# Kernel tuning notes

Measured on AMD Instinct MI355X. Metric: run time of the kernel, lower is better.

The kernel has to match this reference:

```python
import jax, jax.numpy as jnp
import numpy as np

B, N, K, L, H = 8, 2048, 16, 4, 8
CONV = (64, 64, 128, 256)
W_DIM, N_CODES, E_DIM, P_DIM, FF = 512, 8, 64, 256, 512


def act(x):
    return jax.nn.leaky_relu(x, 0.2)


def ln(x, g, b, eps=1e-5):
    m = jnp.mean(x, -1, keepdims=True)
    v = jnp.mean((x - m) ** 2, -1, keepdims=True)
    return g * (x - m) / jnp.sqrt(v + eps) + b


# per-batch neighbor gather: f [C,N], i [N,K] -> [C,N,K]
gather_nb = jax.vmap(lambda f, i: f[:, i])


def knn_idx(y):  # y [B,3,N] -> [B,N,K]
    xx = jnp.sum(y * y, axis=1)
    inner = jnp.einsum('bcn,bcm->bnm', y, y)
    dist = 2.0 * inner - xx[:, :, None] - xx[:, None, :]  # negative sq dist
    return jax.lax.top_k(dist, K)[1]


def mha(q, kv, Wq, bq, Wk, bk, Wv, bv, Wo, bo):
    Bq, S, D = q.shape
    Sk = kv.shape[1]
    dh = D // H
    qh = (q @ Wq.T + bq).reshape(Bq, S, H, dh)
    kh = (kv @ Wk.T + bk).reshape(Bq, Sk, H, dh)
    vh = (kv @ Wv.T + bv).reshape(Bq, Sk, H, dh)
    a = jax.nn.softmax(jnp.einsum('bqhd,bkhd->bhqk', qh, kh) * (1.0 / np.sqrt(dh)))
    o = jnp.einsum('bhqk,bkhd->bqhd', a, vh).reshape(Bq, S, D)
    return o @ Wo.T + bo


def setup_inputs() -> dict:
    key = jax.random.key(0)
    ks = iter(jax.random.split(key, 48))
    nrm = lambda shape: jax.random.normal(next(ks), shape, jnp.float32) * 0.02
    d = {
        'x': jax.random.normal(next(ks), (B, N, 3), jnp.float32),
        'W_ec': nrm((CONV[0], 6)), 'b_ec': jnp.zeros((CONV[0],), jnp.float32),
        'Wc1': nrm((CONV[1], CONV[0])), 'bc1': jnp.zeros((CONV[1],), jnp.float32),
        'Wc2': nrm((CONV[2], CONV[1])), 'bc2': jnp.zeros((CONV[2],), jnp.float32),
        'Wc3': nrm((CONV[3], CONV[2])), 'bc3': jnp.zeros((CONV[3],), jnp.float32),
        'Wf': nrm((W_DIM, sum(CONV))), 'bf': jnp.zeros((W_DIM,), jnp.float32),
        'Wpc': nrm((P_DIM, E_DIM)), 'bpc': jnp.zeros((P_DIM,), jnp.float32),
        'Wpi': nrm((P_DIM, 3)), 'bpi': jnp.zeros((P_DIM,), jnp.float32),
        'Wq': nrm((L, 2, P_DIM, P_DIM)), 'bq': jnp.zeros((L, 2, P_DIM), jnp.float32),
        'Wk': nrm((L, 2, P_DIM, P_DIM)), 'bk': jnp.zeros((L, 2, P_DIM), jnp.float32),
        'Wv': nrm((L, 2, P_DIM, P_DIM)), 'bv': jnp.zeros((L, 2, P_DIM), jnp.float32),
        'Wo': nrm((L, 2, P_DIM, P_DIM)), 'bo': jnp.zeros((L, 2, P_DIM), jnp.float32),
        'ln1g': jnp.ones((L, P_DIM), jnp.float32), 'ln1b': jnp.zeros((L, P_DIM), jnp.float32),
        'ln2g': jnp.ones((L, P_DIM), jnp.float32), 'ln2b': jnp.zeros((L, P_DIM), jnp.float32),
        'Wff1': nrm((L, FF, P_DIM)), 'bff1': jnp.zeros((L, FF), jnp.float32),
        'Wff2': nrm((L, P_DIM, FF)), 'bff2': jnp.zeros((L, P_DIM), jnp.float32),
        'ln3g': jnp.ones((L, P_DIM), jnp.float32), 'ln3b': jnp.zeros((L, P_DIM), jnp.float32),
        'lnfg': jnp.ones((P_DIM,), jnp.float32), 'lnfb': jnp.zeros((P_DIM,), jnp.float32),
        'Wcm': nrm((E_DIM, P_DIM)), 'bcm': jnp.zeros((E_DIM,), jnp.float32),
    }
    return d


def reference(x, W_ec, b_ec, Wc1, bc1, Wc2, bc2, Wc3, bc3, Wf, bf, Wpc, bpc, Wpi, bpi,
              Wq, bq, Wk, bk, Wv, bv, Wo, bo, ln1g, ln1b, ln2g, ln2b,
              Wff1, bff1, Wff2, bff2, ln3g, ln3b, lnfg, lnfb, Wcm, bcm):
    y = jnp.transpose(x, (0, 2, 1))                      # [B,3,N]
    idx = knn_idx(y)                                     # [B,N,K]
    nb = gather_nb(y, idx)                               # [B,3,N,K]
    feats = jnp.concatenate([nb - y[..., None], jnp.broadcast_to(y[..., None], nb.shape)], axis=1)
    h = act(jnp.einsum('oc,bcnk->bonk', W_ec, feats) + b_ec[:, None, None])
    h = h.max(axis=3)                                    # [B,64,N]
    xs = [h]
    for Wl, bl in ((Wc1, bc1), (Wc2, bc2), (Wc3, bc3)):
        h = gather_nb(h, idx).max(axis=3)                # graph max pooling
        h = act(jnp.einsum('oc,bcn->bon', Wl, h) + bl[:, None])
        xs.append(h)
    h = jnp.concatenate(xs, axis=1)                      # [B,512,N]
    h = jnp.einsum('oc,bcn->bon', Wf, h) + bf[:, None]
    xm = h.max(axis=2)                                   # [B,512]
    q = act(xm.reshape(B, N_CODES, E_DIM) @ Wpc.T + bpc) # [B,8,256]
    mem = act(x @ Wpi.T + bpi)                           # [B,N,256]
    for l in range(L):
        q = ln(q + mha(q, q, Wq[l, 0], bq[l, 0], Wk[l, 0], bk[l, 0], Wv[l, 0], bv[l, 0], Wo[l, 0], bo[l, 0]), ln1g[l], ln1b[l])
        q = ln(q + mha(q, mem, Wq[l, 1], bq[l, 1], Wk[l, 1], bk[l, 1], Wv[l, 1], bv[l, 1], Wo[l, 1], bo[l, 1]), ln2g[l], ln2b[l])
        q = ln(q + (act(q @ Wff1[l].T + bff1[l]) @ Wff2[l].T + bff2[l]), ln3g[l], ln3b[l])
    q = ln(q, lnfg, lnfb)
    out = q @ Wcm.T + bcm                                # [B,8,64]
    return out.reshape(B, W_DIM)
```

## Files before the change

### kernel.cpp

```cpp
#include <hip/hip_runtime.h>
#include <math.h>

#define BN 8
#define NP 2048
#define KNN 16
#define NL 4
#define NH 8

typedef __attribute__((ext_vector_type(8))) short bf16x8;
typedef __attribute__((ext_vector_type(4))) float f32x4;

__device__ __forceinline__ unsigned short f2bf(float f) {
    unsigned u = __float_as_uint(f);
    unsigned r = (u + 0x7FFFu + ((u >> 16) & 1u)) >> 16;
    return (unsigned short)r;
}
__device__ __forceinline__ float bf2f(unsigned short s) {
    return __uint_as_float(((unsigned)s) << 16);
}
__device__ __forceinline__ unsigned fmono(float f) {
    unsigned u = __float_as_uint(f);
    return (u & 0x80000000u) ? ~u : (u | 0x80000000u);
}
__device__ __forceinline__ float funmono(unsigned k) {
    return (k & 0x80000000u) ? __uint_as_float(k ^ 0x80000000u) : __uint_as_float(~k);
}


__device__ __forceinline__ unsigned long long shflx_u64(unsigned long long v, int j) {
    int lo = __shfl_xor((int)(unsigned)(v & 0xFFFFFFFFull), j);
    int hi = __shfl_xor((int)(unsigned)(v >> 32), j);
    return ((unsigned long long)(unsigned)hi << 32) | (unsigned)lo;
}

__device__ __forceinline__ unsigned sort64_u32(unsigned v, int lane) {
    #pragma unroll
    for (int k = 2; k <= 64; k <<= 1) {
        #pragma unroll
        for (int j = k >> 1; j > 0; j >>= 1) {
            unsigned o = (unsigned)__shfl_xor((int)v, j);
            bool up = ((lane & k) == 0);
            bool lower = ((lane & j) == 0);
            unsigned mn = v < o ? v : o;
            unsigned mx = v < o ? o : v;
            v = (up == lower) ? mn : mx;
        }
    }
    return v;
}

__device__ __forceinline__ unsigned long long sort64_u64(unsigned long long v, int lane) {
    #pragma unroll
    for (int k = 2; k <= 64; k <<= 1) {
        #pragma unroll
        for (int j = k >> 1; j > 0; j >>= 1) {
            unsigned long long o = shflx_u64(v, j);
            bool up = ((lane & k) == 0);
            bool lower = ((lane & j) == 0);
            unsigned long long mn = v < o ? v : o;
            unsigned long long mx = v < o ? o : v;
            v = (up == lower) ? mn : mx;
        }
    }
    return v;
}

__global__ __launch_bounds__(256) void knn_kernel(const float* __restrict__ x, int* __restrict__ idxout) {
    __shared__ unsigned long long cand[4][64];
    int tid = threadIdx.x;
    int wv = tid >> 6, lane = tid & 63;
    int p = blockIdx.x * 4 + wv;
    int b = p >> 11, n = p & 2047;
    const float* xb = x + (size_t)b * NP * 3;
    float cx = xb[n * 3 + 0], cy = xb[n * 3 + 1], cz = xb[n * 3 + 2];
    float xn = cx * cx + cy * cy + cz * cz;
    unsigned key[32];
    unsigned lmax = 0u;
    #pragma unroll
    for (int t = 0; t < 32; ++t) {
        int m = (t << 6) | lane;
        float mx = xb[m * 3 + 0], my = xb[m * 3 + 1], mz = xb[m * 3 + 2];
        float xxm = mx * mx + my * my + mz * mz;
        float inner = cx * mx + cy * my + cz * mz;
        float dd = 2.0f * inner - xn - xxm;
        unsigned u = __float_as_uint(dd);
        u = (u & 0x80000000u) ? ~u : (u | 0x80000000u);
        key[t] = u;
        lmax = lmax > u ? lmax : u;
    }
    unsigned sorted = sort64_u32(lmax, lane);
    unsigned S = (unsigned)__shfl((int)sorted, 48);
    int c = 0;
    #pragma unroll
    for (int t = 0; t < 32; ++t) c += (key[t] >= S) ? 1 : 0;
    int inc = c;
    #pragma unroll
    for (int d = 1; d < 64; d <<= 1) {
        int tsh = __shfl_up(inc, d);
        if (lane >= d) inc += tsh;
    }
    int C = __shfl(inc, 63);
    int* op = idxout + (size_t)p * KNN;
    if (C <= 64) {
        int off = inc - c;
        #pragma unroll
        for (int t = 0; t < 32; ++t) {
            if (key[t] >= S) {
                int m = (t << 6) | lane;
                cand[wv][off++] = ((unsigned long long)key[t] << 16) | (unsigned)(2047 - m);
            }
        }
        asm volatile("s_waitcnt lgkmcnt(0)" ::: "memory");
        unsigned long long ck = (lane < C) ? cand[wv][lane] : 0ull;
        ck = sort64_u64(ck, lane);
        if (lane >= 48) op[63 - lane] = 2047 - (int)(unsigned)(ck & 0xFFFFull);
    } else {
        unsigned taken = 0u;
        for (int r = 0; r < KNN; ++r) {
            unsigned long long best = 0ull;
            #pragma unroll
            for (int t = 0; t < 32; ++t) {
                if (!((taken >> t) & 1u)) {
                    int m = (t << 6) | lane;
                    unsigned long long ck = ((unsigned long long)key[t] << 16) | (unsigned)(2047 - m);
                    if (ck > best) best = ck;
                }
            }
            #pragma unroll
            for (int d = 1; d < 64; d <<= 1) {
                unsigned long long o = shflx_u64(best, d);
                if (o > best) best = o;
            }
            int m = 2047 - (int)(unsigned)(best & 0xFFFFull);
            if (lane == 0) op[r] = m;
            if ((m & 63) == lane) taken |= 1u << (m >> 6);
        }
    }
}

__global__ __launch_bounds__(256) void edge_conv_kernel(const float* __restrict__ x, const int* __restrict__ idx,
                                                        const float* __restrict__ Wec, const float* __restrict__ bec,
                                                        unsigned short* __restrict__ hcatT) {
    int tid = threadIdx.x;
    int g = tid >> 6, o = tid & 63;
    int p = blockIdx.x * 4 + g;
    int b = p >> 11;
    __shared__ float nb[4][KNN][3];
    __shared__ float ctr[4][3];
    if (o < KNN) {
        int j = idx[(size_t)p * KNN + o];
        const float* xp = x + ((size_t)b * NP + j) * 3;
        nb[g][o][0] = xp[0]; nb[g][o][1] = xp[1]; nb[g][o][2] = xp[2];
    }
    if (o >= KNN && o < KNN + 3) ctr[g][o - KNN] = x[(size_t)p * 3 + (o - KNN)];
    __syncthreads();
    float w0 = Wec[o * 6 + 0], w1 = Wec[o * 6 + 1], w2 = Wec[o * 6 + 2];
    float w3 = Wec[o * 6 + 3], w4 = Wec[o * 6 + 4], w5 = Wec[o * 6 + 5];
    float c0 = ctr[g][0], c1 = ctr[g][1], c2 = ctr[g][2];
    float base = bec[o] + w3 * c0 + w4 * c1 + w5 * c2;
    float m = -3.4e38f;
    #pragma unroll
    for (int k = 0; k < KNN; ++k) {
        float v = base + w0 * (nb[g][k][0] - c0) + w1 * (nb[g][k][1] - c1) + w2 * (nb[g][k][2] - c2);
        v = v > 0.f ? v : 0.2f * v;
        m = fmaxf(m, v);
    }
    hcatT[(size_t)p * 512 + o] = f2bf(m);
}

__global__ __launch_bounds__(256) void pool_bf16_kernel(const unsigned short* __restrict__ src, int s_coff,
                                                        const int* __restrict__ idx,
                                                        unsigned short* __restrict__ dst, int C) {
    int tid = threadIdx.x, wv = tid >> 6, lane = tid & 63;
    int p = blockIdx.x * 4 + wv;
    int b = p >> 11;
    const int* ip = idx + (size_t)p * KNN;
    const unsigned short* sb = src + (size_t)b * NP * 512 + s_coff;
    for (int c0 = 0; c0 < C; c0 += 64) {
        int ch = c0 + lane;
        float m = -3.4e38f;
// ... 102 lines not shown
                                                        const unsigned short* __restrict__ B, size_t b_bstride,
                                                        const float* __restrict__ bias, int bias_per_m,
                                                        void* __restrict__ C, size_t c_bstride, int c_rstride,
                                                        int K, int act, int out_bf16,
                                                        unsigned* __restrict__ xmk, int domax) {
    __shared__ unsigned short As[128][40];
    __shared__ unsigned short Bs[128][40];
    int m0 = blockIdx.x * 128, n0 = blockIdx.y * 128, b = blockIdx.z;
    int tid = threadIdx.x;
    int lane = tid & 63, wave = tid >> 6;
    int wr = wave >> 1, wc = wave & 1;
    int quad = lane >> 4, l16 = lane & 15;
    int r0 = tid >> 2, kc0 = (tid & 3) * 8;
    f32x4 acc[4][4] = {};
    const unsigned short* Ab = A + (size_t)b * a_bstride;
    const unsigned short* Bb = B + (size_t)b * b_bstride;
    for (int k0 = 0; k0 < K; k0 += 32) {
        uint4 a0 = *(const uint4*)(Ab + (size_t)(m0 + r0) * K + k0 + kc0);
        uint4 a1 = *(const uint4*)(Ab + (size_t)(m0 + r0 + 64) * K + k0 + kc0);
        uint4 b0 = *(const uint4*)(Bb + (size_t)(n0 + r0) * K + k0 + kc0);
        uint4 b1 = *(const uint4*)(Bb + (size_t)(n0 + r0 + 64) * K + k0 + kc0);
        __syncthreads();
        *(uint4*)&As[r0][kc0] = a0;
        *(uint4*)&As[r0 + 64][kc0] = a1;
        *(uint4*)&Bs[r0][kc0] = b0;
        *(uint4*)&Bs[r0 + 64][kc0] = b1;
        __syncthreads();
        bf16x8 af[4], bfv[4];
        #pragma unroll
        for (int i = 0; i < 4; ++i) af[i] = *(const bf16x8*)&As[wr * 64 + i * 16 + l16][quad * 8];
        #pragma unroll
        for (int j = 0; j < 4; ++j) bfv[j] = *(const bf16x8*)&Bs[wc * 64 + j * 16 + l16][quad * 8];
        #pragma unroll
        for (int i = 0; i < 4; ++i)
            #pragma unroll
            for (int j = 0; j < 4; ++j)
                acc[i][j] = __builtin_amdgcn_mfma_f32_16x16x32_bf16(af[i], bfv[j], acc[i][j], 0, 0, 0);
    }
    if (domax) {
        #pragma unroll
        for (int i = 0; i < 4; ++i) {
            #pragma unroll
            for (int r = 0; r < 4; ++r) {
                int m = m0 + wr * 64 + i * 16 + quad * 4 + r;
                float v = fmaxf(fmaxf(acc[i][0][r], acc[i][1][r]), fmaxf(acc[i][2][r], acc[i][3][r]));
                v += bias[m];
                #pragma unroll
                for (int off = 1; off <= 8; off <<= 1) v = fmaxf(v, __shfl_xor(v, off));
                if (l16 == 0) atomicMax(&xmk[(size_t)b * 512 + m], fmono(v));
            }
        }
        return;
    }
    #pragma unroll
    for (int i = 0; i < 4; ++i) {
        #pragma unroll
        for (int r = 0; r < 4; ++r) {
            int m = m0 + wr * 64 + i * 16 + quad * 4 + r;
            float bm = bias_per_m ? bias[m] : 0.f;
            #pragma unroll
            for (int j = 0; j < 4; ++j) {
                int n = n0 + wc * 64 + j * 16 + l16;
                float v = acc[i][j][r] + (bias_per_m ? bm : bias[n]);
                if (act) v = v > 0.f ? v : 0.2f * v;
                size_t off = (size_t)b * c_bstride + (size_t)m * c_rstride + n;
                if (out_bf16) ((unsigned short*)C)[off] = f2bf(v);
                else          ((float*)C)[off] = v;
            }
        }
    }
}

__global__ __launch_bounds__(256) void mfma_kv_all_kernel(const unsigned short* __restrict__ A,
                                                          const unsigned short* __restrict__ W,
                                                          const float* __restrict__ bkv,
                                                          unsigned short* __restrict__ KVall) {
    __shared__ unsigned short As[128][40];
    __shared__ unsigned short Bs[128][40];
    int m0 = blockIdx.x * 128;
    int nb = blockIdx.y & 3, l = blockIdx.y >> 2;
    int n0 = nb * 128;
    int b = blockIdx.z;
    int tid = threadIdx.x;
    int lane = tid & 63, wave = tid >> 6;
    int wr = wave >> 1, wc = wave & 1;
    int quad = lane >> 4, l16 = lane & 15;
    int r0 = tid >> 2, kc0 = (tid & 3) * 8;
    f32x4 acc[4][4] = {};
    const unsigned short* Ab = A + (size_t)b * NP * 256;
    const unsigned short* Bb = W + (size_t)l * 131072;
    const float* bias = bkv + l * 512;
    for (int k0 = 0; k0 < 256; k0 += 32) {
        uint4 a0 = *(const uint4*)(Ab + (size_t)(m0 + r0) * 256 + k0 + kc0);
        uint4 a1 = *(const uint4*)(Ab + (size_t)(m0 + r0 + 64) * 256 + k0 + kc0);
        uint4 b0 = *(const uint4*)(Bb + (size_t)(n0 + r0) * 256 + k0 + kc0);
        uint4 b1 = *(const uint4*)(Bb + (size_t)(n0 + r0 + 64) * 256 + k0 + kc0);
        __syncthreads();
        *(uint4*)&As[r0][kc0] = a0;
        *(uint4*)&As[r0 + 64][kc0] = a1;
        *(uint4*)&Bs[r0][kc0] = b0;
        *(uint4*)&Bs[r0 + 64][kc0] = b1;
        __syncthreads();
        bf16x8 af[4], bfv[4];
        #pragma unroll
        for (int i = 0; i < 4; ++i) af[i] = *(const bf16x8*)&As[wr * 64 + i * 16 + l16][quad * 8];
        #pragma unroll
        for (int j = 0; j < 4; ++j) bfv[j] = *(const bf16x8*)&Bs[wc * 64 + j * 16 + l16][quad * 8];
        #pragma unroll
        for (int i = 0; i < 4; ++i)
            #pragma unroll
            for (int j = 0; j < 4; ++j)
                acc[i][j] = __builtin_amdgcn_mfma_f32_16x16x32_bf16(af[i], bfv[j], acc[i][j], 0, 0, 0);
    }
    unsigned short* Cb = KVall + ((size_t)l * BN + b) * NP * 512;
    #pragma unroll
    for (int i = 0; i < 4; ++i) {
        #pragma unroll
        for (int r = 0; r < 4; ++r) {
            int m = m0 + wr * 64 + i * 16 + quad * 4 + r;
            #pragma unroll
            for (int j = 0; j < 4; ++j) {
                int n = n0 + wc * 64 + j * 16 + l16;
                Cb[(size_t)m * 512 + n] = f2bf(acc[i][j][r] + bias[n]);
            }
        }
    }
}

__global__ __launch_bounds__(256) void pc_kernel(const unsigned* __restrict__ xmk, const float* __restrict__ Wpc,
                                                 const float* __restrict__ bpc, float* __restrict__ q) {
    int id = blockIdx.x * 256 + threadIdx.x;
    int p = id & 255;
    int rowi = id >> 8;
    int b = rowi >> 3, i = rowi & 7;
    const unsigned* xr = xmk + b * 512 + i * 64;
    const float* w = Wpc + (size_t)p * 64;
    float acc = bpc[p];
    #pragma unroll
    for (int e = 0; e < 64; ++e) acc += funmono(xr[e]) * w[e];
    q[id] = acc > 0.f ? acc : 0.2f * acc;
}

__global__ __launch_bounds__(256) void mem_kernel(const float* __restrict__ x, const float* __restrict__ Wpi,
                                                  const float* __restrict__ bpi, unsigned short* __restrict__ memB) {
    size_t id = (size_t)blockIdx.x * 256 + threadIdx.x;
    int p = (int)(id & 255);
    size_t pt = id >> 8;
    float x0 = x[pt * 3 + 0], x1 = x[pt * 3 + 1], x2 = x[pt * 3 + 2];
    float v = bpi[p] + x0 * Wpi[p * 3 + 0] + x1 * Wpi[p * 3 + 1] + x2 * Wpi[p * 3 + 2];
    v = v > 0.f ? v : 0.2f * v;
    memB[id] = f2bf(v);
}

__global__ __launch_bounds__(256) void qkv_proj_kernel(const float* __restrict__ in,
                                                       const float* __restrict__ Wq0, const float* __restrict__ bq0,
                                                       const float* __restrict__ Wk0, const float* __restrict__ bk0,
                                                       const float* __restrict__ Wv0, const float* __restrict__ bv0,
                                                       float* __restrict__ Qs, float* __restrict__ Ks,
                                                       float* __restrict__ Vs) {
    int which = blockIdx.y;
    const float* W = (which == 0) ? Wq0 : (which == 1) ? Wk0 : Wv0;
    const float* bb = (which == 0) ? bq0 : (which == 1) ? bk0 : bv0;
    float* out = (which == 0) ? Qs : (which == 1) ? Ks : Vs;
    __shared__ __align__(16) float r[256];
    int row = blockIdx.x, tid = threadIdx.x;
    r[tid] = in[(size_t)row * 256 + tid];
    __syncthreads();
    const float4* w4 = (const float4*)(W + (size_t)tid * 256);
    const float4* r4 = (const float4*)r;
    float acc = bb[tid];
    #pragma unroll 8
    for (int c = 0; c < 64; ++c) {
        float4 a = r4[c], wv = w4[c];
        acc += a.x * wv.x + a.y * wv.y + a.z * wv.z + a.w * wv.w;
    }
    out[(size_t)row * 256 + tid] = acc;
}

__global__ __launch_bounds__(256) void attn_ln_kernel(const float* __restrict__ Qs, const float* __restrict__ Ks,
                                                      const float* __restrict__ Vs, const float* __restrict__ Wo,
                                                      const float* __restrict__ bo, const float* __restrict__ res,
                                                      const float* __restrict__ g, const float* __restrict__ bt,
                                                      const float* __restrict__ Wq1, const float* __restrict__ bq1,
                                                      float* __restrict__ out, float* __restrict__ Qc) {
    int row = blockIdx.x, tid = threadIdx.x;
    int b = row >> 3;
    __shared__ float Kl[2048], Vl[2048], qr[256];
    __shared__ float sc[64];
    __shared__ __align__(16) float r[256];
    __shared__ __align__(16) float aout[256];
    __shared__ float red[256];
    for (int t = tid; t < 2048; t += 256) {
        Kl[t] = Ks[(size_t)b * 2048 + t];
        Vl[t] = Vs[(size_t)b * 2048 + t];
    }
    qr[tid] = Qs[(size_t)row * 256 + tid];
    __syncthreads();
    const float scale = 0.17677669529663687f;
    if (tid < 64) {
        int h = tid >> 3, k = tid & 7;
        float dot = 0.f;
        #pragma unroll
        for (int d = 0; d < 32; ++d) dot += qr[h * 32 + d] * Kl[k * 256 + h * 32 + d];
        sc[tid] = dot * scale;
    }
    __syncthreads();
    if (tid < 8) {
        float* p = sc + tid * 8;
        float m = -3.4e38f;
        #pragma unroll
        for (int k = 0; k < 8; ++k) m = fmaxf(m, p[k]);
        float s = 0.f;
        #pragma unroll
        for (int k = 0; k < 8; ++k) { p[k] = __expf(p[k] - m); s += p[k]; }
        float inv = 1.f / s;
        #pragma unroll
        for (int k = 0; k < 8; ++k) p[k] *= inv;
    }
    __syncthreads();
    {
        int h = tid >> 5;
        float acc = 0.f;
        #pragma unroll
        for (int k = 0; k < 8; ++k) acc += sc[h * 8 + k] * Vl[k * 256 + tid];
        r[tid] = acc;
    }
    __syncthreads();
    const float4* w4 = (const float4*)(Wo + (size_t)tid * 256);
    const float4* r4 = (const float4*)r;
    float acc = bo[tid];
    #pragma unroll 8
    for (int c = 0; c < 64; ++c) {
        float4 a = r4[c], wv = w4[c];
        acc += a.x * wv.x + a.y * wv.y + a.z * wv.z + a.w * wv.w;
    }
    float v = res[(size_t)row * 256 + tid] + acc;
    red[tid] = v; __syncthreads();
    for (int s = 128; s; s >>= 1) { if (tid < s) red[tid] += red[tid + s]; __syncthreads(); }
    float mean = red[0] * (1.0f / 256.0f);
    __syncthreads();
    float dv = v - mean;
    red[tid] = dv * dv; __syncthreads();
    for (int s = 128; s; s >>= 1) { if (tid < s) red[tid] += red[tid + s]; __syncthreads(); }
    float var = red[0] * (1.0f / 256.0f);
    float oln = g[tid] * dv * rsqrtf(var + 1e-5f) + bt[tid];
    out[(size_t)row * 256 + tid] = oln;
    aout[tid] = oln;
    __syncthreads();
    {
        const float4* wq4 = (const float4*)(Wq1 + (size_t)tid * 256);
        const float4* a4 = (const float4*)aout;
        float qacc = bq1[tid];
        #pragma unroll 8
        for (int c = 0; c < 64; ++c) {
            float4 a = a4[c], wv = wq4[c];
            qacc += a.x * wv.x + a.y * wv.y + a.z * wv.z + a.w * wv.w;
        }
        Qc[(size_t)row * 256 + tid] = qacc;
    }
}

__global__ __launch_bounds__(256) void ca_part_kernel(const float* __restrict__ Qc,
                                                      const unsigned short* __restrict__ KVl,
                                                      float* __restrict__ part) {
    int kb = blockIdx.x, h = blockIdx.y, b = blockIdx.z;
    int tid = threadIdx.x;
    __shared__ float q[8][32];
    __shared__ __align__(16) float S[8][128];
    __shared__ float om[8][8][32];
    const float scale = 0.17677669529663687f;
    {
        int i = tid >> 5, d = tid & 31;
        q[i][d] = Qc[(size_t)(b * 8 + i) * 256 + h * 32 + d];
    }
    __syncthreads();
    {
        int kk = tid & 127, half = tid >> 7;
        int k = kb * 128 + kk;
        const unsigned short* kp = KVl + ((size_t)b * NP + k) * 512 + h * 32;
        float kd[32];
        #pragma unroll
        for (int u = 0; u < 4; ++u) {
            uint4 raw = *(const uint4*)(kp + u * 8);
            unsigned w0 = raw.x, w1 = raw.y, w2 = raw.z, w3 = raw.w;
            kd[u * 8 + 0] = __uint_as_float(w0 << 16); kd[u * 8 + 1] = __uint_as_float(w0 & 0xFFFF0000u);
            kd[u * 8 + 2] = __uint_as_float(w1 << 16); kd[u * 8 + 3] = __uint_as_float(w1 & 0xFFFF0000u);
            kd[u * 8 + 4] = __uint_as_float(w2 << 16); kd[u * 8 + 5] = __uint_as_float(w2 & 0xFFFF0000u);
            kd[u * 8 + 6] = __uint_as_float(w3 << 16); kd[u * 8 + 7] = __uint_as_float(w3 & 0xFFFF0000u);
        }
        #pragma unroll
        for (int i = 0; i < 4; ++i) {
            int ri = half * 4 + i;
            float dot = 0.f;
            #pragma unroll
            for (int d = 0; d < 32; ++d) dot += q[ri][d] * kd[d];
            S[ri][kk] = dot * scale;
        }
    }
    __syncthreads();
    float* pout = part + (((size_t)(b * NH + h)) * 16 + kb) * 288;
    {
        int i = tid >> 5, l32 = tid & 31;
        float m = -3.4e38f;
        #pragma unroll
        for (int t = 0; t < 4; ++t) m = fmaxf(m, S[i][l32 + t * 32]);
        #pragma unroll
        for (int off = 16; off; off >>= 1) m = fmaxf(m, __shfl_xor(m, off));
        float s = 0.f;
        #pragma unroll
        for (int t = 0; t < 4; ++t) {
            float e = __expf(S[i][l32 + t * 32] - m);
            S[i][l32 + t * 32] = e;
            s += e;
        }
        #pragma unroll
        for (int off = 16; off; off >>= 1) s += __shfl_xor(s, off);
        if (l32 == 0) { pout[i] = m; pout[8 + i] = s; }
    }
    __syncthreads();
    {
        int d = tid & 31, grp = tid >> 5;
        const unsigned short* Vb = KVl + ((size_t)b * NP + kb * 128) * 512 + 256 + h * 32 + d;
        float acc[8] = {};
        #pragma unroll 4
        for (int t = 0; t < 16; ++t) {
            int kk = grp * 16 + t;
            float v = bf2f(Vb[(size_t)kk * 512]);
            #pragma unroll
            for (int i = 0; i < 8; ++i) acc[i] += S[i][kk] * v;
        }
        #pragma unroll
        for (int i = 0; i < 8; ++i) om[grp][i][d] = acc[i];
    }
    __syncthreads();
    {
        int i = tid >> 5, d = tid & 31;
        float sum = 0.f;
        #pragma unroll
        for (int g = 0; g < 8; ++g) sum += om[g][i][d];
        pout[16 + i * 32 + d] = sum;
    }
}

__global__ __launch_bounds__(256) void combine_ff_kernel(const float* __restrict__ part, const float* __restrict__ Wo,
                                                         const float* __restrict__ bo, const float* __restrict__ res,
                                                         const float* __restrict__ g2, const float* __restrict__ b2t,
                                                         const float* __restrict__ W1, const float* __restrict__ b1,
                                                         const float* __restrict__ W2, const float* __restrict__ b2,
                                                         const float* __restrict__ g3, const float* __restrict__ b3t,
                                                         float* __restrict__ out,
                                                         int is_last, const float* __restrict__ lnfg,
                                                         const float* __restrict__ lnfb, const float* __restrict__ Wcm,
                                                         const float* __restrict__ bcm, float* __restrict__ finout) {
    int row = blockIdx.x, tid = threadIdx.x;
    int b = row >> 3, i = row & 7;
    __shared__ __align__(16) float r[256];
    __shared__ __align__(16) float a[256];
    __shared__ __align__(16) float hbuf[512];
    __shared__ float red[256];
    {
        int h = tid >> 5, d = tid & 31;
        const float* pb = part + (size_t)(b * NH + h) * 16 * 288;
        float M = -3.4e38f;
        #pragma unroll
        for (int kb = 0; kb < 16; ++kb) M = fmaxf(M, pb[kb * 288 + i]);
        float L = 0.f, O = 0.f;
        #pragma unroll
        for (int kb = 0; kb < 16; ++kb) {
            float w = __expf(pb[kb * 288 + i] - M);
            L += pb[kb * 288 + 8 + i] * w;
            O += pb[kb * 288 + 16 + i * 32 + d] * w;
        }
        r[tid] = O / L;
    }
    __syncthreads();
    {
        const float4* w4 = (const float4*)(Wo + (size_t)tid * 256);
        const float4* r4 = (const float4*)r;
        float acc = bo[tid];
        #pragma unroll 8
        for (int c = 0; c < 64; ++c) {
            float4 av = r4[c], wv = w4[c];
            acc += av.x * wv.x + av.y * wv.y + av.z * wv.z + av.w * wv.w;
        }
        float v = res[(size_t)row * 256 + tid] + acc;
        red[tid] = v; __syncthreads();
        for (int s = 128; s; s >>= 1) { if (tid < s) red[tid] += red[tid + s]; __syncthreads(); }
        float mean = red[0] * (1.0f / 256.0f);
        __syncthreads();
        float dv = v - mean;
        red[tid] = dv * dv; __syncthreads();
        for (int s = 128; s; s >>= 1) { if (tid < s) red[tid] += red[tid + s]; __syncthreads(); }
        float var = red[0] * (1.0f / 256.0f);
        a[tid] = g2[tid] * dv * rsqrtf(var + 1e-5f) + b2t[tid];
    }
    __syncthreads();
    {
        const float4* a4 = (const float4*)a;
        #pragma unroll
        for (int half = 0; half < 2; ++half) {
            int o = tid + half * 256;
            const float4* w4 = (const float4*)(W1 + (size_t)o * 256);
            float acc = b1[o];
            #pragma unroll 8
            for (int c = 0; c < 64; ++c) {
                float4 av = a4[c], wv = w4[c];
                acc += av.x * wv.x + av.y * wv.y + av.z * wv.z + av.w * wv.w;
            }
            hbuf[o] = acc > 0.f ? acc : 0.2f * acc;
        }
    }
    __syncthreads();
    float tln;
    {
        const float4* h4 = (const float4*)hbuf;
        const float4* w4 = (const float4*)(W2 + (size_t)tid * 512);
        float acc = b2[tid];
        #pragma unroll 8
        for (int c = 0; c < 128; ++c) {
            float4 av = h4[c], wv = w4[c];
            acc += av.x * wv.x + av.y * wv.y + av.z * wv.z + av.w * wv.w;
        }
        float v = a[tid] + acc;
        red[tid] = v; __syncthreads();
        for (int s = 128; s; s >>= 1) { if (tid < s) red[tid] += red[tid + s]; __syncthreads(); }
        float mean = red[0] * (1.0f / 256.0f);
        __syncthreads();
        float dv = v - mean;
        red[tid] = dv * dv; __syncthreads();
        for (int s = 128; s; s >>= 1) { if (tid < s) red[tid] += red[tid + s]; __syncthreads(); }
        float var = red[0] * (1.0f / 256.0f);
        tln = g3[tid] * dv * rsqrtf(var + 1e-5f) + b3t[tid];
    }
    if (!is_last) {
        out[(size_t)row * 256 + tid] = tln;
        return;
    }
    __syncthreads();
    red[tid] = tln; __syncthreads();
    for (int s = 128; s; s >>= 1) { if (tid < s) red[tid] += red[tid + s]; __syncthreads(); }
    float mean = red[0] * (1.0f / 256.0f);
    __syncthreads();
    float dv = tln - mean;
    red[tid] = dv * dv; __syncthreads();
    for (int s = 128; s; s >>= 1) { if (tid < s) red[tid] += red[tid + s]; __syncthreads(); }
    float var = red[0] * (1.0f / 256.0f);
    a[tid] = lnfg[tid] * dv * rsqrtf(var + 1e-5f) + lnfb[tid];
    __syncthreads();
    if (tid < 64) {
        const float4* w4 = (const float4*)(Wcm + (size_t)tid * 256);
        const float4* a4 = (const float4*)a;
        float acc = bcm[tid];
        #pragma unroll 8
        for (int c = 0; c < 64; ++c) {
            float4 av = a4[c], wv = w4[c];
            acc += av.x * wv.x + av.y * wv.y + av.z * wv.z + av.w * wv.w;
        }
        finout[(size_t)b * 512 + i * 64 + tid] = acc;
    }
}

extern "C" void kernel_launch(void* const* d_in, const int* in_sizes, int n_in,
                              void* d_out, int out_size, void* d_ws, size_t ws_size,
                              hipStream_t stream) {
    const float* x    = (const float*)d_in[0];
    const float* Wec  = (const float*)d_in[1];
    const float* bec  = (const float*)d_in[2];
    const float* Wc1  = (const float*)d_in[3];
    const float* bc1  = (const float*)d_in[4];
    const float* Wc2  = (const float*)d_in[5];
    const float* bc2  = (const float*)d_in[6];
    const float* Wc3  = (const float*)d_in[7];
    const float* bc3  = (const float*)d_in[8];
    const float* Wf   = (const float*)d_in[9];
    const float* bf   = (const float*)d_in[10];
    const float* Wpc  = (const float*)d_in[11];
    const float* bpc  = (const float*)d_in[12];
    const float* Wpi  = (const float*)d_in[13];
    const float* bpi  = (const float*)d_in[14];
    const float* Wq   = (const float*)d_in[15];
    const float* bq   = (const float*)d_in[16];
    const float* Wk   = (const float*)d_in[17];
    const float* bk   = (const float*)d_in[18];
    const float* Wv   = (const float*)d_in[19];
    const float* bv   = (const float*)d_in[20];
    const float* Wo   = (const float*)d_in[21];
    const float* bo   = (const float*)d_in[22];
    const float* ln1g = (const float*)d_in[23];
    const float* ln1b = (const float*)d_in[24];
    const float* ln2g = (const float*)d_in[25];
    const float* ln2b = (const float*)d_in[26];
    const float* Wff1 = (const float*)d_in[27];
    const float* bff1 = (const float*)d_in[28];
    const float* Wff2 = (const float*)d_in[29];
    const float* bff2 = (const float*)d_in[30];
    const float* ln3g = (const float*)d_in[31];
    const float* ln3b = (const float*)d_in[32];
    const float* lnfg = (const float*)d_in[33];
    const float* lnfb = (const float*)d_in[34];
    const float* Wcm  = (const float*)d_in[35];
    const float* bcm  = (const float*)d_in[36];
    float* out = (float*)d_out;

    float* ws = (float*)d_ws;
    size_t off = 0;
    auto alloc = [&](size_t n) { float* p = ws + off; off += (n + 3) & ~(size_t)3; return p; };
    int*            idx   = (int*)alloc((size_t)BN * NP * KNN);
    unsigned short* hcatT = (unsigned short*)alloc((size_t)BN * NP * 512 / 2);
    unsigned short* poolT = (unsigned short*)alloc((size_t)BN * NP * 128 / 2);
    unsigned short* WfB   = (unsigned short*)alloc(262144 / 2);
    unsigned short* Wc1B  = (unsigned short*)alloc(4096 / 2);
    unsigned short* Wc2B  = (unsigned short*)alloc(8192 / 2);
    unsigned short* Wc3B  = (unsigned short*)alloc(32768 / 2);
    unsigned short* WkvB  = (unsigned short*)alloc(524288 / 2);
    float*          bkv   = alloc(2048);
    unsigned short* memB  = (unsigned short*)alloc((size_t)BN * NP * 256 / 2);
    unsigned short* KVall = (unsigned short*)alloc((size_t)NL * BN * NP * 512 / 2);
    unsigned*       xmk   = (unsigned*)alloc((size_t)BN * 512);
    float*          qa    = alloc((size_t)BN * 8 * 256);
    float*          qb    = alloc((size_t)BN * 8 * 256);
    float*          Qs    = alloc((size_t)BN * 8 * 256);
    float*          Ks    = alloc((size_t)BN * 8 * 256);
    float*          Vs    = alloc((size_t)BN * 8 * 256);
    float*          Qc    = alloc((size_t)BN * 8 * 256);
    float*          part  = alloc((size_t)BN * NH * 16 * 288);

    wcast_kernel<<<3272, 256, 0, stream>>>(Wf, Wc3, Wk, Wv, bk, bv, Wc1, Wc2,
                                           WfB, Wc3B, WkvB, bkv, Wc1B, Wc2B, xmk);

    knn_kernel<<<BN * NP / 4, 256, 0, stream>>>(x, idx);
    edge_conv_kernel<<<BN * NP / 4, 256, 0, stream>>>(x, idx, Wec, bec, hcatT);

    pool_bf16_kernel<<<BN * NP / 4, 256, 0, stream>>>(hcatT, 0, idx, poolT, 64);
    mfma_conv64_kernel<<<dim3(NP / 128, 1, BN), 256, 0, stream>>>(poolT, Wc1B, bc1, hcatT, 64);
    pool_bf16_kernel<<<BN * NP / 4, 256, 0, stream>>>(hcatT, 64, idx, poolT, 64);
    mfma_gemm_kernel<<<dim3(NP / 128, 1, BN), 256, 0, stream>>>(poolT, (size_t)NP * 64, Wc2B, 0,
                                                                bc2, 0, (void*)(hcatT + 128), (size_t)NP * 512, 512,
                                                                64, 1, 1, nullptr, 0);
    pool_bf16_kernel<<<BN * NP / 4, 256, 0, stream>>>(hcatT, 128, idx, poolT, 128);
    mfma_gemm_kernel<<<dim3(NP / 128, 2, BN), 256, 0, stream>>>(poolT, (size_t)NP * 128, Wc3B, 0,
                                                                bc3, 0, (void*)(hcatT + 256), (size_t)NP * 512, 512,
                                                                128, 1, 1, nullptr, 0);
    mfma_gemm_kernel<<<dim3(4, NP / 128, BN), 256, 0, stream>>>(WfB, 0, hcatT, (size_t)NP * 512,
                                                                bf, 1, nullptr, 0, 0,
                                                                512, 0, 0, xmk, 1);
    pc_kernel<<<BN * 8, 256, 0, stream>>>(xmk, Wpc, bpc, qa);
    mem_kernel<<<BN * NP, 256, 0, stream>>>(x, Wpi, bpi, memB);
    mfma_kv_all_kernel<<<dim3(NP / 128, 4 * NL, BN), 256, 0, stream>>>(memB, WkvB, bkv, KVall);

    float* qcur = qa; float* qnxt = qb;
    for (int l = 0; l < NL; ++l) {
        const float* Wq0 = Wq + (size_t)(l * 2 + 0) * 65536; const float* bq0 = bq + (l * 2 + 0) * 256;
        const float* Wk0 = Wk + (size_t)(l * 2 + 0) * 65536; const float* bk0 = bk + (l * 2 + 0) * 256;
        const float* Wv0 = Wv + (size_t)(l * 2 + 0) * 65536; const float* bv0 = bv + (l * 2 + 0) * 256;
        const float* Wo0 = Wo + (size_t)(l * 2 + 0) * 65536; const float* bo0 = bo + (l * 2 + 0) * 256;
        const float* Wq1 = Wq + (size_t)(l * 2 + 1) * 65536; const float* bq1 = bq + (l * 2 + 1) * 256;
        const float* Wo1 = Wo + (size_t)(l * 2 + 1) * 65536; const float* bo1 = bo + (l * 2 + 1) * 256;
        int last = (l == NL - 1);

        qkv_proj_kernel<<<dim3(BN * 8, 3), 256, 0, stream>>>(qcur, Wq0, bq0, Wk0, bk0, Wv0, bv0, Qs, Ks, Vs);
        attn_ln_kernel<<<BN * 8, 256, 0, stream>>>(Qs, Ks, Vs, Wo0, bo0, qcur,
                                                   ln1g + l * 256, ln1b + l * 256, Wq1, bq1, qnxt, Qc);
        ca_part_kernel<<<dim3(16, NH, BN), 256, 0, stream>>>(Qc, KVall + (size_t)l * BN * NP * 512, part);
        combine_ff_kernel<<<BN * 8, 256, 0, stream>>>(part, Wo1, bo1, qnxt,
                                                      ln2g + l * 256, ln2b + l * 256,
                                                      Wff1 + (size_t)l * 512 * 256, bff1 + l * 512,
                                                      Wff2 + (size_t)l * 256 * 512, bff2 + l * 256,
                                                      ln3g + l * 256, ln3b + l * 256, qcur,
                                                      last, lnfg, lnfb, Wcm, bcm, out);
    }

    (void)in_sizes; (void)n_in; (void)out_size; (void)ws_size; (void)qnxt;
}
```

Baseline: 615.6 us.

## Restructure transformer tail into split-bf16 MFMA GEMM kernels with LN folding

Replaces the per-row scalar matvec kernels of the decoder (QKV projection, attention plus LN, combine plus FFN) with a generic 64-row MFMA GEMM kernel. The kernel uses a hi/lo bf16 split to keep near-fp32 accuracy and folds the preceding LayerNorm into its input load. Each weight matrix is now read once per panel instead of once per row, which cuts the redundant weight traffic of the 64-block matvec design. The cost is many more small launches per layer (about eight instead of four), each using only 4-12 blocks, plus extra global round trips for intermediates.

```diff
diff --git a/kernel.cpp b/kernel.cpp
--- a/kernel.cpp
+++ b/kernel.cpp
@@ -9,6 +9,7 @@
 
 typedef __attribute__((ext_vector_type(8))) short bf16x8;
 typedef __attribute__((ext_vector_type(4))) float f32x4;
+typedef __attribute__((ext_vector_type(4))) unsigned short us4;
 
 __device__ __forceinline__ unsigned short f2bf(float f) {
     unsigned u = __float_as_uint(f);
@@ -25,7 +26,6 @@
 __device__ __forceinline__ float funmono(unsigned k) {
     return (k & 0x80000000u) ? __uint_as_float(k ^ 0x80000000u) : __uint_as_float(~k);
 }
-
 
 __device__ __forceinline__ unsigned long long shflx_u64(unsigned long long v, int j) {
     int lo = __shfl_xor((int)(unsigned)(v & 0xFFFFFFFFull), j);
@@ -434,61 +434,150 @@
     memB[id] = f2bf(v);
 }
 
-__global__ __launch_bounds__(256) void qkv_proj_kernel(const float* __restrict__ in,
-                                                       const float* __restrict__ Wq0, const float* __restrict__ bq0,
-                                                       const float* __restrict__ Wk0, const float* __restrict__ bk0,
-                                                       const float* __restrict__ Wv0, const float* __restrict__ bv0,
-                                                       float* __restrict__ Qs, float* __restrict__ Ks,
-                                                       float* __restrict__ Vs) {
-    int which = blockIdx.y;
-    const float* W = (which == 0) ? Wq0 : (which == 1) ? Wk0 : Wv0;
-    const float* bb = (which == 0) ? bq0 : (which == 1) ? bk0 : bv0;
-    float* out = (which == 0) ? Qs : (which == 1) ? Ks : Vs;
-    __shared__ __align__(16) float r[256];
-    int row = blockIdx.x, tid = threadIdx.x;
-    r[tid] = in[(size_t)row * 256 + tid];
-    __syncthreads();
-    const float4* w4 = (const float4*)(W + (size_t)tid * 256);
-    const float4* r4 = (const float4*)r;
-    float acc = bb[tid];
-    #pragma unroll 8
-    for (int c = 0; c < 64; ++c) {
-        float4 a = r4[c], wv = w4[c];
-        acc += a.x * wv.x + a.y * wv.y + a.z * wv.z + a.w * wv.w;
-    }
-    out[(size_t)row * 256 + tid] = acc;
-}
-
-__global__ __launch_bounds__(256) void attn_ln_kernel(const float* __restrict__ Qs, const float* __restrict__ Ks,
-                                                      const float* __restrict__ Vs, const float* __restrict__ Wo,
-                                                      const float* __restrict__ bo, const float* __restrict__ res,
-                                                      const float* __restrict__ g, const float* __restrict__ bt,
-                                                      const float* __restrict__ Wq1, const float* __restrict__ bq1,
-                                                      float* __restrict__ out, float* __restrict__ Qc) {
-    int row = blockIdx.x, tid = threadIdx.x;
-    int b = row >> 3;
-    __shared__ float Kl[2048], Vl[2048], qr[256];
-    __shared__ float sc[64];
-    __shared__ __align__(16) float r[256];
-    __shared__ __align__(16) float aout[256];
-    __shared__ float red[256];
-    for (int t = tid; t < 2048; t += 256) {
-        Kl[t] = Ks[(size_t)b * 2048 + t];
-        Vl[t] = Vs[(size_t)b * 2048 + t];
-    }
-    qr[tid] = Qs[(size_t)row * 256 + tid];
+__global__ __launch_bounds__(256) void tail_gemm_kernel(
+    const float* __restrict__ in, int K, int nk,
+    const float* __restrict__ Wa, const float* __restrict__ Wb2, const float* __restrict__ Wc2,
+    const float* __restrict__ ba, const float* __restrict__ bb2, const float* __restrict__ bc2,
+    const float* __restrict__ resid,
+    const float* __restrict__ lng, const float* __restrict__ lnb, float* __restrict__ lnout,
+    float* __restrict__ out, int N, int act)
+{
+    __shared__ unsigned short Ah[64][72], Al[64][72];
+    __shared__ unsigned short Bh[64][72], Bl[64][72];
+    __shared__ float meanv[64], rsv[64];
+    int panel = blockIdx.x;
+    int tid = threadIdx.x;
+    int lane = tid & 63, w = tid >> 6;
+    int quad = lane >> 4, l16 = lane & 15;
+    int grp = panel >> 2;
+    const float* W = (grp == 0) ? Wa : (grp == 1) ? Wb2 : Wc2;
+    const float* bi = (grp == 0) ? ba : (grp == 1) ? bb2 : bc2;
+    int row_base = (panel & 3) * 64;
+    int fold = (lng != nullptr);
+    int wrln = (lnout != nullptr) && (panel == 0);
+
+    if (fold) {
+        for (int j = 0; j < 16; ++j) {
+            int row = w * 16 + j;
+            float4 xv = *(const float4*)(in + (size_t)row * 256 + lane * 4);
+            float s = xv.x + xv.y + xv.z + xv.w;
+            float s2 = xv.x * xv.x + xv.y * xv.y + xv.z * xv.z + xv.w * xv.w;
+            #pragma unroll
+            for (int o = 1; o < 64; o <<= 1) { s += __shfl_xor(s, o); s2 += __shfl_xor(s2, o); }
+            if (lane == 0) {
+                float mean = s * (1.0f / 256.0f);
+                float var = s2 * (1.0f / 256.0f) - mean * mean;
+                meanv[row] = mean;
+                rsv[row] = rsqrtf(var + 1e-5f);
+            }
+        }
+        __syncthreads();
+    }
+
+    f32x4 acc[4] = {};
+    int r = tid >> 2, cb = (tid & 3) * 16;
+    for (int c = 0; c < nk; ++c) {
+        {
+            const float* src = in + (size_t)r * K + c * 64 + cb;
+            float mean = 0.f, rs = 1.f;
+            if (fold) { mean = meanv[r]; rs = rsv[r]; }
+            #pragma unroll
+            for (int u = 0; u < 4; ++u) {
+                float4 xv = *(const float4*)(src + u * 4);
+                float n0, n1, n2, n3;
+                if (fold) {
+                    int gcol = c * 64 + cb + u * 4;
+                    float4 g4 = *(const float4*)(lng + gcol);
+                    float4 b4 = *(const float4*)(lnb + gcol);
+                    n0 = g4.x * (xv.x - mean) * rs + b4.x;
+                    n1 = g4.y * (xv.y - mean) * rs + b4.y;
+                    n2 = g4.z * (xv.z - mean) * rs + b4.z;
+                    n3 = g4.w * (xv.w - mean) * rs + b4.w;
+                    if (wrln) *(float4*)(lnout + (size_t)r * 256 + gcol) = make_float4(n0, n1, n2, n3);
+                } else {
+                    n0 = xv.x; n1 = xv.y; n2 = xv.z; n3 = xv.w;
+                }
+                us4 hv, lv;
+                hv[0] = f2bf(n0); lv[0] = f2bf(n0 - bf2f(hv[0]));
+                hv[1] = f2bf(n1); lv[1] = f2bf(n1 - bf2f(hv[1]));
+                hv[2] = f2bf(n2); lv[2] = f2bf(n2 - bf2f(hv[2]));
+                hv[3] = f2bf(n3); lv[3] = f2bf(n3 - bf2f(hv[3]));
+                *(us4*)&Ah[r][cb + u * 4] = hv;
+                *(us4*)&Al[r][cb + u * 4] = lv;
+            }
+        }
+        {
+            const float* srcw = W + (size_t)(row_base + r) * K + c * 64 + cb;
+            #pragma unroll
+            for (int u = 0; u < 4; ++u) {
+                float4 wv2 = *(const float4*)(srcw + u * 4);
+                us4 hv, lv;
+                hv[0] = f2bf(wv2.x); lv[0] = f2bf(wv2.x - bf2f(hv[0]));
+                hv[1] = f2bf(wv2.y); lv[1] = f2bf(wv2.y - bf2f(hv[1]));
+                hv[2] = f2bf(wv2.z); lv[2] = f2bf(wv2.z - bf2f(hv[2]));
+                hv[3] = f2bf(wv2.w); lv[3] = f2bf(wv2.w - bf2f(hv[3]));
+                *(us4*)&Bh[r][cb + u * 4] = hv;
+                *(us4*)&Bl[r][cb + u * 4] = lv;
+            }
+        }
+        __syncthreads();
+        #pragma unroll
+        for (int k0 = 0; k0 < 64; k0 += 32) {
+            bf16x8 ah[4], alo[4];
+            #pragma unroll
+            for (int i = 0; i < 4; ++i) {
+                ah[i] = *(const bf16x8*)&Ah[i * 16 + l16][k0 + quad * 8];
+                alo[i] = *(const bf16x8*)&Al[i * 16 + l16][k0 + quad * 8];
+            }
+            bf16x8 bh = *(const bf16x8*)&Bh[w * 16 + l16][k0 + quad * 8];
+            bf16x8 bl = *(const bf16x8*)&Bl[w * 16 + l16][k0 + quad * 8];
+            #pragma unroll
+            for (int i = 0; i < 4; ++i) {
+                acc[i] = __builtin_amdgcn_mfma_f32_16x16x32_bf16(ah[i], bh, acc[i], 0, 0, 0);
+                acc[i] = __builtin_amdgcn_mfma_f32_16x16x32_bf16(ah[i], bl, acc[i], 0, 0, 0);
+                acc[i] = __builtin_amdgcn_mfma_f32_16x16x32_bf16(alo[i], bh, acc[i], 0, 0, 0);
+            }
+        }
+        __syncthreads();
+    }
+    int cl = w * 16 + l16;
+    int n = panel * 64 + cl;
+    float bv = bi[row_base + cl];
+    #pragma unroll
+    for (int i = 0; i < 4; ++i) {
+        #pragma unroll
+        for (int r_ = 0; r_ < 4; ++r_) {
+            int m = i * 16 + quad * 4 + r_;
+            float v = acc[i][r_] + bv;
+            if (act) v = v > 0.f ? v : 0.2f * v;
+            if (resid) v += resid[(size_t)m * N + n];
+            out[(size_t)m * N + n] = v;
+        }
+    }
+}
+
+__global__ __launch_bounds__(256) void sattn_kernel(const float* __restrict__ QKV, float* __restrict__ ao) {
+    int b = blockIdx.x, tid = threadIdx.x;
+    __shared__ __align__(16) float q[8][768];
+    __shared__ float sc[8][64];
+    const float* src = QKV + (size_t)b * 8 * 768;
+    for (int t = tid; t < 8 * 768 / 4; t += 256)
+        ((float4*)&q[0][0])[t] = ((const float4*)src)[t];
     __syncthreads();
     const float scale = 0.17677669529663687f;
+    #pragma unroll
+    for (int u = 0; u < 2; ++u) {
+        int idx = u * 256 + tid;
+        int i = idx >> 6, h = (idx >> 3) & 7, k = idx & 7;
+        float dot = 0.f;
+        #pragma unroll
+        for (int d = 0; d < 32; ++d) dot += q[i][h * 32 + d] * q[k][256 + h * 32 + d];
+        sc[i][h * 8 + k] = dot * scale;
+    }
+    __syncthreads();
     if (tid < 64) {
-        int h = tid >> 3, k = tid & 7;
-        float dot = 0.f;
-        #pragma unroll
-        for (int d = 0; d < 32; ++d) dot += qr[h * 32 + d] * Kl[k * 256 + h * 32 + d];
-        sc[tid] = dot * scale;
-    }
-    __syncthreads();
-    if (tid < 8) {
-        float* p = sc + tid * 8;
+        int i = tid >> 3, h = tid & 7;
+        float* p = &sc[i][h * 8];
         float m = -3.4e38f;
         #pragma unroll
         for (int k = 0; k < 8; ++k) m = fmaxf(m, p[k]);
@@ -501,44 +590,14 @@
     }
     __syncthreads();
     {
-        int h = tid >> 5;
-        float acc = 0.f;
-        #pragma unroll
-        for (int k = 0; k < 8; ++k) acc += sc[h * 8 + k] * Vl[k * 256 + tid];
-        r[tid] = acc;
-    }
-    __syncthreads();
-    const float4* w4 = (const float4*)(Wo + (size_t)tid * 256);
-    const float4* r4 = (const float4*)r;
-    float acc = bo[tid];
-    #pragma unroll 8
-    for (int c = 0; c < 64; ++c) {
-        float4 a = r4[c], wv = w4[c];
-        acc += a.x * wv.x + a.y * wv.y + a.z * wv.z + a.w * wv.w;
-    }
-    float v = res[(size_t)row * 256 + tid] + acc;
-    red[tid] = v; __syncthreads();
-    for (int s = 128; s; s >>= 1) { if (tid < s) red[tid] += red[tid + s]; __syncthreads(); }
-    float mean = red[0] * (1.0f / 256.0f);
-    __syncthreads();
-    float dv = v - mean;
-    red[tid] = dv * dv; __syncthreads();
-    for (int s = 128; s; s >>= 1) { if (tid < s) red[tid] += red[tid + s]; __syncthreads(); }
-    float var = red[0] * (1.0f / 256.0f);
-    float oln = g[tid] * dv * rsqrtf(var + 1e-5f) + bt[tid];
-    out[(size_t)row * 256 + tid] = oln;
-    aout[tid] = oln;
-    __syncthreads();
-    {
-        const float4* wq4 = (const float4*)(Wq1 + (size_t)tid * 256);
-        const float4* a4 = (const float4*)aout;
-        float qacc = bq1[tid];
-        #pragma unroll 8
-        for (int c = 0; c < 64; ++c) {
-            float4 a = a4[c], wv = wq4[c];
-            qacc += a.x * wv.x + a.y * wv.y + a.z * wv.z + a.w * wv.w;
-        }
-        Qc[(size_t)row * 256 + tid] = qacc;
+        int h = tid >> 5, d = tid & 31;
+        #pragma unroll
+        for (int i = 0; i < 8; ++i) {
+            float acc = 0.f;
+            #pragma unroll
+            for (int k = 0; k < 8; ++k) acc += sc[i][h * 8 + k] * q[k][512 + h * 32 + d];
+            ao[((size_t)b * 8 + i) * 256 + h * 32 + d] = acc;
+        }
     }
 }
 
@@ -624,110 +683,53 @@
     }
 }
 
-__global__ __launch_bounds__(256) void combine_ff_kernel(const float* __restrict__ part, const float* __restrict__ Wo,
-                                                         const float* __restrict__ bo, const float* __restrict__ res,
-                                                         const float* __restrict__ g2, const float* __restrict__ b2t,
-                                                         const float* __restrict__ W1, const float* __restrict__ b1,
-                                                         const float* __restrict__ W2, const float* __restrict__ b2,
-                                                         const float* __restrict__ g3, const float* __restrict__ b3t,
-                                                         float* __restrict__ out,
-                                                         int is_last, const float* __restrict__ lnfg,
-                                                         const float* __restrict__ lnfb, const float* __restrict__ Wcm,
-                                                         const float* __restrict__ bcm, float* __restrict__ finout) {
+__global__ __launch_bounds__(256) void comb_kernel(const float* __restrict__ part, float* __restrict__ r) {
     int row = blockIdx.x, tid = threadIdx.x;
     int b = row >> 3, i = row & 7;
-    __shared__ __align__(16) float r[256];
+    int h = tid >> 5, d = tid & 31;
+    const float* pb = part + (size_t)(b * NH + h) * 16 * 288;
+    float M = -3.4e38f;
+    #pragma unroll
+    for (int kb = 0; kb < 16; ++kb) M = fmaxf(M, pb[kb * 288 + i]);
+    float L = 0.f, O = 0.f;
+    #pragma unroll
+    for (int kb = 0; kb < 16; ++kb) {
+        float w = __expf(pb[kb * 288 + i] - M);
+        L += pb[kb * 288 + 8 + i] * w;
+        O += pb[kb * 288 + 16 + i * 32 + d] * w;
+    }
+    r[(size_t)row * 256 + tid] = O / L;
+}
+
+__global__ __launch_bounds__(256) void lfin_kernel(const float* __restrict__ t3,
+                                                   const float* __restrict__ g3, const float* __restrict__ b3,
+                                                   const float* __restrict__ lnfg, const float* __restrict__ lnfb,
+                                                   const float* __restrict__ Wcm, const float* __restrict__ bcm,
+                                                   float* __restrict__ out) {
+    int row = blockIdx.x, tid = threadIdx.x;
+    int b = row >> 3, i = row & 7;
+    __shared__ float red[256];
     __shared__ __align__(16) float a[256];
-    __shared__ __align__(16) float hbuf[512];
-    __shared__ float red[256];
-    {
-        int h = tid >> 5, d = tid & 31;
-        const float* pb = part + (size_t)(b * NH + h) * 16 * 288;
-        float M = -3.4e38f;
-        #pragma unroll
-        for (int kb = 0; kb < 16; ++kb) M = fmaxf(M, pb[kb * 288 + i]);
-        float L = 0.f, O = 0.f;
-        #pragma unroll
-        for (int kb = 0; kb < 16; ++kb) {
-            float w = __expf(pb[kb * 288 + i] - M);
-            L += pb[kb * 288 + 8 + i] * w;
-            O += pb[kb * 288 + 16 + i * 32 + d] * w;
-        }
-        r[tid] = O / L;
-    }
-    __syncthreads();
-    {
-        const float4* w4 = (const float4*)(Wo + (size_t)tid * 256);
-        const float4* r4 = (const float4*)r;
-        float acc = bo[tid];
-        #pragma unroll 8
-        for (int c = 0; c < 64; ++c) {
-            float4 av = r4[c], wv = w4[c];
-            acc += av.x * wv.x + av.y * wv.y + av.z * wv.z + av.w * wv.w;
-        }
-        float v = res[(size_t)row * 256 + tid] + acc;
-        red[tid] = v; __syncthreads();
-        for (int s = 128; s; s >>= 1) { if (tid < s) red[tid] += red[tid + s]; __syncthreads(); }
-        float mean = red[0] * (1.0f / 256.0f);
-        __syncthreads();
-        float dv = v - mean;
-        red[tid] = dv * dv; __syncthreads();
-        for (int s = 128; s; s >>= 1) { if (tid < s) red[tid] += red[tid + s]; __syncthreads(); }
-        float var = red[0] * (1.0f / 256.0f);
-        a[tid] = g2[tid] * dv * rsqrtf(var + 1e-5f) + b2t[tid];
-    }
-    __syncthreads();
-    {
-        const float4* a4 = (const float4*)a;
-        #pragma unroll
-        for (int half = 0; half < 2; ++half) {
-            int o = tid + half * 256;
-            const float4* w4 = (const float4*)(W1 + (size_t)o * 256);
-            float acc = b1[o];
-            #pragma unroll 8
-            for (int c = 0; c < 64; ++c) {
-                float4 av = a4[c], wv = w4[c];
-                acc += av.x * wv.x + av.y * wv.y + av.z * wv.z + av.w * wv.w;
-            }
-            hbuf[o] = acc > 0.f ? acc : 0.2f * acc;
-        }
-    }
-    __syncthreads();
-    float tln;
-    {
-        const float4* h4 = (const float4*)hbuf;
-        const float4* w4 = (const float4*)(W2 + (size_t)tid * 512);
-        float acc = b2[tid];
-        #pragma unroll 8
-        for (int c = 0; c < 128; ++c) {
-            float4 av = h4[c], wv = w4[c];
-            acc += av.x * wv.x + av.y * wv.y + av.z * wv.z + av.w * wv.w;
-        }
-        float v = a[tid] + acc;
-        red[tid] = v; __syncthreads();
-        for (int s = 128; s; s >>= 1) { if (tid < s) red[tid] += red[tid + s]; __syncthreads(); }
-        float mean = red[0] * (1.0f / 256.0f);
-        __syncthreads();
-        float dv = v - mean;
-        red[tid] = dv * dv; __syncthreads();
-        for (int s = 128; s; s >>= 1) { if (tid < s) red[tid] += red[tid + s]; __syncthreads(); }
-        float var = red[0] * (1.0f / 256.0f);
-        tln = g3[tid] * dv * rsqrtf(var + 1e-5f) + b3t[tid];
-    }
-    if (!is_last) {
-        out[(size_t)row * 256 + tid] = tln;
-        return;
-    }
-    __syncthreads();
-    red[tid] = tln; __syncthreads();
+    float v = t3[(size_t)row * 256 + tid];
+    red[tid] = v; __syncthreads();
     for (int s = 128; s; s >>= 1) { if (tid < s) red[tid] += red[tid + s]; __syncthreads(); }
     float mean = red[0] * (1.0f / 256.0f);
     __syncthreads();
-    float dv = tln - mean;
+    float dv = v - mean;
     red[tid] = dv * dv; __syncthreads();
     for (int s = 128; s; s >>= 1) { if (tid < s) red[tid] += red[tid + s]; __syncthreads(); }
     float var = red[0] * (1.0f / 256.0f);
-    a[tid] = lnfg[tid] * dv * rsqrtf(var + 1e-5f) + lnfb[tid];
+    float tln = g3[tid] * dv * rsqrtf(var + 1e-5f) + b3[tid];
+    __syncthreads();
+    red[tid] = tln; __syncthreads();
+    for (int s = 128; s; s >>= 1) { if (tid < s) red[tid] += red[tid + s]; __syncthreads(); }
+    float mean2 = red[0] * (1.0f / 256.0f);
+    __syncthreads();
+    float d2 = tln - mean2;
+    red[tid] = d2 * d2; __syncthreads();
+    for (int s = 128; s; s >>= 1) { if (tid < s) red[tid] += red[tid + s]; __syncthreads(); }
+    float var2 = red[0] * (1.0f / 256.0f);
+    a[tid] = lnfg[tid] * d2 * rsqrtf(var2 + 1e-5f) + lnfb[tid];
     __syncthreads();
     if (tid < 64) {
         const float4* w4 = (const float4*)(Wcm + (size_t)tid * 256);
@@ -738,7 +740,7 @@
             float4 av = a4[c], wv = w4[c];
             acc += av.x * wv.x + av.y * wv.y + av.z * wv.z + av.w * wv.w;
         }
-        finout[(size_t)b * 512 + i * 64 + tid] = acc;
+        out[(size_t)b * 512 + i * 64 + tid] = acc;
     }
 }
 
@@ -800,11 +802,17 @@
     unsigned short* KVall = (unsigned short*)alloc((size_t)NL * BN * NP * 512 / 2);
     unsigned*       xmk   = (unsigned*)alloc((size_t)BN * 512);
     float*          qa    = alloc((size_t)BN * 8 * 256);
-    float*          qb    = alloc((size_t)BN * 8 * 256);
-    float*          Qs    = alloc((size_t)BN * 8 * 256);
-    float*          Ks    = alloc((size_t)BN * 8 * 256);
-    float*          Vs    = alloc((size_t)BN * 8 * 256);
+    float*          QKVb  = alloc((size_t)BN * 8 * 768);
+    float*          ao    = alloc((size_t)BN * 8 * 256);
+    float*          t1    = alloc((size_t)BN * 8 * 256);
+    float*          q1    = alloc((size_t)BN * 8 * 256);
     float*          Qc    = alloc((size_t)BN * 8 * 256);
+    float*          t2    = alloc((size_t)BN * 8 * 256);
+    float*          aln   = alloc((size_t)BN * 8 * 256);
+    float*          hb    = alloc((size_t)BN * 8 * 512);
+    float*          t3b   = alloc((size_t)BN * 8 * 256);
+    float*          rb    = alloc((size_t)BN * 8 * 256);
+    float*          qcb   = alloc((size_t)BN * 8 * 256);
     float*          part  = alloc((size_t)BN * NH * 16 * 288);
 
     wcast_kernel<<<3272, 256, 0, stream>>>(Wf, Wc3, Wk, Wv, bk, bv, Wc1, Wc2,
@@ -830,7 +838,6 @@
     mem_kernel<<<BN * NP, 256, 0, stream>>>(x, Wpi, bpi, memB);
     mfma_kv_all_kernel<<<dim3(NP / 128, 4 * NL, BN), 256, 0, stream>>>(memB, WkvB, bkv, KVall);
 
-    float* qcur = qa; float* qnxt = qb;
     for (int l = 0; l < NL; ++l) {
         const float* Wq0 = Wq + (size_t)(l * 2 + 0) * 65536; const float* bq0 = bq + (l * 2 + 0) * 256;
         const float* Wk0 = Wk + (size_t)(l * 2 + 0) * 65536; const float* bk0 = bk + (l * 2 + 0) * 256;
@@ -838,19 +845,36 @@
         const float* Wo0 = Wo + (size_t)(l * 2 + 0) * 65536; const float* bo0 = bo + (l * 2 + 0) * 256;
         const float* Wq1 = Wq + (size_t)(l * 2 + 1) * 65536; const float* bq1 = bq + (l * 2 + 1) * 256;
         const float* Wo1 = Wo + (size_t)(l * 2 + 1) * 65536; const float* bo1 = bo + (l * 2 + 1) * 256;
-        int last = (l == NL - 1);
-
-        qkv_proj_kernel<<<dim3(BN * 8, 3), 256, 0, stream>>>(qcur, Wq0, bq0, Wk0, bk0, Wv0, bv0, Qs, Ks, Vs);
-        attn_ln_kernel<<<BN * 8, 256, 0, stream>>>(Qs, Ks, Vs, Wo0, bo0, qcur,
-                                                   ln1g + l * 256, ln1b + l * 256, Wq1, bq1, qnxt, Qc);
+        const float* W1  = Wff1 + (size_t)l * 131072; const float* b1 = bff1 + l * 512;
+        const float* W2  = Wff2 + (size_t)l * 131072; const float* b2 = bff2 + l * 256;
+
+        const float* qin;
+        const float* qcur;
+        if (l == 0) {
+            qin = qa; qcur = qa;
+            tail_gemm_kernel<<<12, 256, 0, stream>>>(qin, 256, 4, Wq0, Wk0, Wv0, bq0, bk0, bv0,
+                                                     nullptr, nullptr, nullptr, nullptr, QKVb, 768, 0);
+        } else {
+            qin = t3b; qcur = qcb;
+            tail_gemm_kernel<<<12, 256, 0, stream>>>(qin, 256, 4, Wq0, Wk0, Wv0, bq0, bk0, bv0,
+                                                     nullptr, ln3g + (l - 1) * 256, ln3b + (l - 1) * 256, qcb,
+                                                     QKVb, 768, 0);
+        }
+        sattn_kernel<<<BN, 256, 0, stream>>>(QKVb, ao);
+        tail_gemm_kernel<<<4, 256, 0, stream>>>(ao, 256, 4, Wo0, nullptr, nullptr, bo0, nullptr, nullptr,
+                                                qcur, nullptr, nullptr, nullptr, t1, 256, 0);
+        tail_gemm_kernel<<<4, 256, 0, stream>>>(t1, 256, 4, Wq1, nullptr, nullptr, bq1, nullptr, nullptr,
+                                                nullptr, ln1g + l * 256, ln1b + l * 256, q1, Qc, 256, 0);
         ca_part_kernel<<<dim3(16, NH, BN), 256, 0, stream>>>(Qc, KVall + (size_t)l * BN * NP * 512, part);
-        combine_ff_kernel<<<BN * 8, 256, 0, stream>>>(part, Wo1, bo1, qnxt,
-                                                      ln2g + l * 256, ln2b + l * 256,
-                                                      Wff1 + (size_t)l * 512 * 256, bff1 + l * 512,
-                                                      Wff2 + (size_t)l * 256 * 512, bff2 + l * 256,
-                                                      ln3g + l * 256, ln3b + l * 256, qcur,
-                                                      last, lnfg, lnfb, Wcm, bcm, out);
-    }
-
-    (void)in_sizes; (void)n_in; (void)out_size; (void)ws_size; (void)qnxt;
-}
+        comb_kernel<<<BN * 8, 256, 0, stream>>>(part, rb);
+        tail_gemm_kernel<<<4, 256, 0, stream>>>(rb, 256, 4, Wo1, nullptr, nullptr, bo1, nullptr, nullptr,
+                                                q1, nullptr, nullptr, nullptr, t2, 256, 0);
+        tail_gemm_kernel<<<8, 256, 0, stream>>>(t2, 256, 4, W1, W1 + 65536, nullptr, b1, b1 + 256, nullptr,
+                                                nullptr, ln2g + l * 256, ln2b + l * 256, aln, hb, 512, 1);
+        tail_gemm_kernel<<<4, 256, 0, stream>>>(hb, 512, 8, W2, nullptr, nullptr, b2, nullptr, nullptr,
+                                                aln, nullptr, nullptr, nullptr, t3b, 256, 0);
+    }
+    lfin_kernel<<<BN * 8, 256, 0, stream>>>(t3b, ln3g + 3 * 256, ln3b + 3 * 256, lnfg, lnfb, Wcm, bcm, out);
+
+    (void)in_sizes; (void)n_in; (void)out_size; (void)ws_size;
+}
```

Measured after the change: 841.4 us. 1.37x slower.
